# Kernel optimization log

Measured on AMD Instinct MI355X. Metric: run time of the kernel, lower is better.

Reference implementation:

```python
import jax, jax.numpy as jnp
import numpy as np

B, T, C = 2, 4096, 768
N_HEAD = 12
HEAD_DIM = C // N_HEAD


def setup_inputs() -> dict:
    key = jax.random.key(0)
    k1, k2, k3, k4, k5 = jax.random.split(key, 5)
    scale = 1.0 / np.sqrt(C)
    x = jax.random.normal(k1, (B, T, C), dtype=jnp.float32)
    # weights stored as [in, out] (transpose of torch Linear weight)
    W_attn = jax.random.normal(k2, (C, 3 * C), dtype=jnp.float32) * scale
    b_attn = jax.random.normal(k3, (3 * C,), dtype=jnp.float32) * 0.01
    W_proj = jax.random.normal(k4, (C, C), dtype=jnp.float32) * scale
    b_proj = jax.random.normal(k5, (C,), dtype=jnp.float32) * 0.01
    return {"x": x, "W_attn": W_attn, "b_attn": b_attn, "W_proj": W_proj, "b_proj": b_proj}


def reference(x, W_attn, b_attn, W_proj, b_proj):
    Bq, Tq, Cq = x.shape
    qkv = x @ W_attn + b_attn                      # [B, T, 3C]
    q, k, v = jnp.split(qkv, 3, axis=-1)           # each [B, T, C]

    def heads(t):
        return t.reshape(Bq, Tq, N_HEAD, HEAD_DIM).transpose(0, 2, 1, 3)  # [B, H, T, D]

    q, k, v = heads(q), heads(k), heads(v)
    att = jnp.einsum('bhqd,bhkd->bhqk', q, k) * (1.0 / np.sqrt(HEAD_DIM))  # [B, H, T, T]
    causal = jnp.tril(jnp.ones((Tq, Tq), dtype=bool))                      # [T, T]
    att = jnp.where(causal[None, None], att, jnp.finfo(att.dtype).min)
    att = jax.nn.softmax(att, axis=-1)
    y = jnp.einsum('bhqk,bhkd->bhqd', att, v)      # [B, H, T, D]
    y = y.transpose(0, 2, 1, 3).reshape(Bq, Tq, Cq)
    return y @ W_proj + b_proj
```

## Files before the change

kernel.cpp:

```cpp
#include <hip/hip_runtime.h>


#define TSEQ   4096
#define NHEAD  12
#define CDIM   768
#define C3     2304
#define BT_TOT 8192

#define PSTR   72

typedef __bf16 bf16x8 __attribute__((ext_vector_type(8)));
typedef __bf16 bf16x2 __attribute__((ext_vector_type(2)));
typedef float  f32x4  __attribute__((ext_vector_type(4)));

__device__ __forceinline__ unsigned short f2bf(float f) {
  unsigned int u = __builtin_bit_cast(unsigned int, f);
  u += 0x7FFFu + ((u >> 16) & 1u);
  return (unsigned short)(u >> 16);
}

__device__ __forceinline__ unsigned int pack2bf(float a, float b) {
  bf16x2 v = {(__bf16)a, (__bf16)b};
  return __builtin_bit_cast(unsigned int, v);
}

__device__ __forceinline__ f32x4 mfma16(bf16x8 a, bf16x8 b, f32x4 c) {
  return __builtin_amdgcn_mfma_f32_16x16x32_bf16(a, b, c, 0, 0, 0);
}

typedef const __attribute__((address_space(1))) void* gas_ptr;
typedef __attribute__((address_space(3))) void* las_ptr;

#define LGKM_WAIT() __builtin_amdgcn_s_waitcnt(0xC07F)


__global__ __launch_bounds__(256) void cast_f32_bf16(const float* __restrict__ x,
                                                     unsigned short* __restrict__ o, int n) {
  int i = (blockIdx.x * 256 + threadIdx.x) * 4;
  if (i < n) {
    float4 v = *(const float4*)(x + i);
    ushort4 u;
    u.x = f2bf(v.x); u.y = f2bf(v.y); u.z = f2bf(v.z); u.w = f2bf(v.w);
    *(ushort4*)(o + i) = u;
  }
}

__global__ __launch_bounds__(256) void transpose_cast(const float* __restrict__ src,
                                                      unsigned short* __restrict__ dst,
                                                      int K, int N) {
  __shared__ float tile[32][33];
  int n0 = blockIdx.x * 32, k0 = blockIdx.y * 32;
  int tx = threadIdx.x, ty = threadIdx.y;
#pragma unroll
  for (int i = 0; i < 4; ++i)
    tile[ty + i * 8][tx] = src[(size_t)(k0 + ty + i * 8) * N + n0 + tx];
  __syncthreads();
#pragma unroll
  for (int i = 0; i < 4; ++i)
    dst[(size_t)(n0 + ty + i * 8) * K + k0 + tx] = f2bf(tile[tx][ty + i * 8]);
}


__device__ __forceinline__ void gemm_bt_mainloop(const unsigned short* __restrict__ A,
                                                 const unsigned short* __restrict__ BTm,
                                                 int K, int m0, int n0,
                                                 unsigned short* lds, f32x4 acc[4][4]) {
  const int tid = threadIdx.x;
  const int wave = tid >> 6, lane = tid & 63;
  const int quad = lane >> 4, l16 = lane & 15;
  const int wm = (wave >> 1) * 64, wn = (wave & 1) * 64;
  const int srow = tid >> 2;
  const int scol = (tid & 3) * 8;

  for (int k0 = 0; k0 < K; k0 += 32) {
    __syncthreads();
#pragma unroll
    for (int r = 0; r < 2; ++r) {
      const unsigned short* ga = A + (size_t)(m0 + r * 64 + srow) * K + k0 + scol;
      __builtin_amdgcn_global_load_lds((gas_ptr)ga,
          (las_ptr)(lds + r * 2048 + wave * 512), 16, 0, 0);
      const unsigned short* gb = BTm + (size_t)(n0 + r * 64 + srow) * K + k0 + scol;
      __builtin_amdgcn_global_load_lds((gas_ptr)gb,
          (las_ptr)(lds + 4096 + r * 2048 + wave * 512), 16, 0, 0);
    }
    __syncthreads();

    bf16x8 af[4], bfr[4];
#pragma unroll
    for (int i = 0; i < 4; ++i) {
      af[i]  = *(const bf16x8*)(lds + (wm + i * 16 + l16) * 32 + quad * 8);
      bfr[i] = *(const bf16x8*)(lds + 4096 + (wn + i * 16 + l16) * 32 + quad * 8);
    }
#pragma unroll
    for (int i = 0; i < 4; ++i)
#pragma unroll
      for (int j = 0; j < 4; ++j)
        acc[i][j] = mfma16(af[i], bfr[j], acc[i][j]);
  }
}

__global__ __launch_bounds__(256) void gemm_qkv_kernel(
    const unsigned short* __restrict__ A, const unsigned short* __restrict__ BTm,
    const float* __restrict__ bias,
    unsigned short* __restrict__ qbuf, unsigned short* __restrict__ kbuf,
    unsigned short* __restrict__ vtbuf) {
  __shared__ __align__(16) unsigned short lds[128 * 136];
  f32x4 zero = {0.f, 0.f, 0.f, 0.f};
  f32x4 acc[4][4];
#pragma unroll
  for (int i = 0; i < 4; ++i)
#pragma unroll
    for (int j = 0; j < 4; ++j) acc[i][j] = zero;

  const int m0 = blockIdx.y * 128, n0 = blockIdx.x * 128;
  gemm_bt_mainloop(A, BTm, CDIM, m0, n0, lds, acc);

  const int tid = threadIdx.x;
  const int wave = tid >> 6, lane = tid & 63;
  const int quad = lane >> 4, l16 = lane & 15;
  const int wm = (wave >> 1) * 64, wn = (wave & 1) * 64;
  const float KSCALE = 0.125f * 1.44269504088896340736f;

  const int seg = n0 / CDIM;
  const float mult = (seg == 1) ? KSCALE : 1.0f;

  __syncthreads();
#pragma unroll
  for (int j = 0; j < 4; ++j) {
    const int nl = wn + j * 16 + l16;
    const float bv = bias[n0 + nl];
#pragma unroll
    for (int i = 0; i < 4; ++i) {
#pragma unroll
      for (int r = 0; r < 4; ++r) {
        const int ml = wm + i * 16 + quad * 4 + r;
        unsigned short val = f2bf((acc[i][j][r] + bv) * mult);
        if (seg < 2) lds[ml * 136 + nl] = val;
        else         lds[nl * 136 + ml] = val;
      }
    }
  }
  __syncthreads();

  const int row = tid >> 1, half = tid & 1;
  const unsigned short* src = lds + row * 136 + half * 64;
  unsigned short* dst;
  if (seg < 2) {
    const int m = m0 + row, b = m >> 12, t = m & (TSEQ - 1);
    const int nn = (n0 - seg * CDIM) + half * 64;
    const int h = nn >> 6;
    unsigned short* base = (seg == 0) ? qbuf : kbuf;
    dst = base + ((size_t)(b * NHEAD + h) * TSEQ + t) * 64;
  } else {
    const int nn = (n0 - 2 * CDIM) + row;
    const int h = nn >> 6, d = nn & 63;
    const int b = m0 >> 12, t0 = (m0 & (TSEQ - 1)) + half * 64;
    dst = vtbuf + ((size_t)(b * NHEAD + h) * 64 + d) * TSEQ + t0;
  }
#pragma unroll
  for (int k = 0; k < 8; ++k)
    *(uint4*)(dst + k * 8) = *(const uint4*)(src + k * 8);
}

__global__ __launch_bounds__(256) void gemm_out_kernel(
    const unsigned short* __restrict__ A, const unsigned short* __restrict__ BTm,
    const float* __restrict__ bias, float* __restrict__ out) {
  __shared__ __align__(16) unsigned short lds[8192];
  f32x4 zero = {0.f, 0.f, 0.f, 0.f};
  f32x4 acc[4][4];
#pragma unroll
  for (int i = 0; i < 4; ++i)
#pragma unroll
    for (int j = 0; j < 4; ++j) acc[i][j] = zero;

  const int m0 = blockIdx.y * 128, n0 = blockIdx.x * 128;
  gemm_bt_mainloop(A, BTm, CDIM, m0, n0, lds, acc);

  const int tid = threadIdx.x;
  const int wave = tid >> 6, lane = tid & 63;
  const int quad = lane >> 4, l16 = lane & 15;
  const int wm = (wave >> 1) * 64, wn = (wave & 1) * 64;

#pragma unroll
  for (int j = 0; j < 4; ++j) {
    int n = n0 + wn + j * 16 + l16;
    float bv = bias[n];
#pragma unroll
    for (int i = 0; i < 4; ++i) {
#pragma unroll
      for (int r = 0; r < 4; ++r) {
        int m = m0 + wm + i * 16 + quad * 4 + r;
        out[(size_t)m * CDIM + n] = acc[i][j][r] + bv;
      }
    }
  }
}


__device__ __forceinline__ void stage_kv4(const unsigned short* __restrict__ Kp,
                                          const unsigned short* __restrict__ Vp,
                                          int j0, unsigned short* kb, unsigned short* vb,
                                          int tid, int wave) {
  const int row = tid >> 3;
  const int col = ((tid & 7) ^ (row & 7)) * 8;
  __builtin_amdgcn_global_load_lds((gas_ptr)(Kp + (size_t)(j0 + row) * 64 + col),
                                   (las_ptr)(kb + wave * 512), 16, 0, 0);
  __builtin_amdgcn_global_load_lds((gas_ptr)(Kp + (size_t)(j0 + 32 + row) * 64 + col),
                                   (las_ptr)(kb + 2048 + wave * 512), 16, 0, 0);
  __builtin_amdgcn_global_load_lds((gas_ptr)(Vp + (size_t)row * TSEQ + j0 + col),
                                   (las_ptr)(vb + wave * 512), 16, 0, 0);
  __builtin_amdgcn_global_load_lds((gas_ptr)(Vp + (size_t)(row + 32) * TSEQ + j0 + col),
                                   (las_ptr)(vb + 2048 + wave * 512), 16, 0, 0);
}

__device__ __forceinline__ void qk_score(const bf16x8 kf[8], const bf16x8 qf[2], f32x4 s[4]) {
  f32x4 zero = {0.f, 0.f, 0.f, 0.f};
#pragma unroll
  for (int i = 0; i < 4; ++i)
    s[i] = mfma16(kf[2 * i + 1], qf[1], mfma16(kf[2 * i], qf[0], zero));
}

template <bool MASKED>
__device__ __forceinline__ void exp_write(const f32x4 s[4], unsigned short* __restrict__ prow,
                                          int j0, int q0, int l16, int quad, float& lsum) {
#pragma unroll
  for (int i = 0; i < 4; ++i) {
    float p[4];
#pragma unroll
    for (int r = 0; r < 4; ++r) {
      p[r] = __builtin_amdgcn_exp2f(s[i][r]);
      if (MASKED) {
        if (j0 + i * 16 + quad * 4 + r > q0 + l16) p[r] = 0.f;
      }
      lsum += p[r];
    }
    uint2 w;
    w.x = pack2bf(p[0], p[1]);
    w.y = pack2bf(p[2], p[3]);
    *(uint2*)(prow + l16 * PSTR + i * 16 + quad * 4) = w;
  }
}

__device__ __forceinline__ void pv8(const unsigned short* __restrict__ vb, int kcol0,
                                    const unsigned short* __restrict__ prow,
                                    int l16, int quad, f32x4 o[4]) {
  bf16x8 pf0 = *(const bf16x8*)(prow + l16 * PSTR + quad * 8);
  bf16x8 pf1 = *(const bf16x8*)(prow + l16 * PSTR + 32 + quad * 8);
#pragma unroll
  for (int dt = 0; dt < 4; ++dt) {
    bf16x8 v0 = *(const bf16x8*)(vb + (16 * dt + l16) * 64 + kcol0);
    bf16x8 v1 = *(const bf16x8*)(vb + (16 * dt + l16) * 64 + (kcol0 ^ 32));
    o[dt] = mfma16(pf1, v1, mfma16(pf0, v0, o[dt]));
  }
}

__global__ __launch_bounds__(256, 3) void attn_kernel(const unsigned short* __restrict__ qbuf,
                                                      const unsigned short* __restrict__ kbuf,
                                                      const unsigned short* __restrict__ vtbuf,
                                                      unsigned short* __restrict__ y) {
  __shared__ __align__(16) unsigned short k_lds[2][64 * 64];
  __shared__ __align__(16) unsigned short v_lds[2][64 * 64];
  __shared__ __align__(16) unsigned short p_lds[4][2][16 * PSTR];

  const int tid = threadIdx.x;
  const int wave = tid >> 6, lane = tid & 63;
  const int quad = lane >> 4, l16 = lane & 15;

  const int bh = blockIdx.x % 24;
  const int p = blockIdx.x / 24;
  const int qA0 = p * 64 + wave * 16;
  const int qB0 = (63 - p) * 64 + wave * 16;

  const unsigned short* Qp = qbuf + (size_t)bh * TSEQ * 64;
  const unsigned short* Kp = kbuf + (size_t)bh * TSEQ * 64;
  const unsigned short* Vp = vtbuf + (size_t)bh * 64 * TSEQ;
  unsigned short* prowA = &p_lds[wave][0][0];
  unsigned short* prowB = &p_lds[wave][1][0];

  bf16x8 qfA[2], qfB[2];
  qfA[0] = *(const bf16x8*)(Qp + (size_t)(qA0 + l16) * 64 + quad * 8);
  qfA[1] = *(const bf16x8*)(Qp + (size_t)(qA0 + l16) * 64 + 32 + quad * 8);
  qfB[0] = *(const bf16x8*)(Qp + (size_t)(qB0 + l16) * 64 + quad * 8);
  qfB[1] = *(const bf16x8*)(Qp + (size_t)(qB0 + l16) * 64 + 32 + quad * 8);

  f32x4 zero = {0.f, 0.f, 0.f, 0.f};
  f32x4 oA[4], oB[4];
#pragma unroll
  for (int dt = 0; dt < 4; ++dt) { oA[dt] = zero; oB[dt] = zero; }
  float lsA = 0.f, lsB = 0.f;

  const int kcol0 = (quad ^ (l16 & 7)) * 8;
  const int ntiles = 64 - p;

  stage_kv4(Kp, Vp, 0, k_lds[0], v_lds[0], tid, wave);

  for (int jt = 0; jt < ntiles; ++jt) {
    __syncthreads();
    if (jt + 1 < ntiles)
      stage_kv4(Kp, Vp, (jt + 1) * 64, k_lds[(jt + 1) & 1], v_lds[(jt + 1) & 1], tid, wave);

    const unsigned short* kb = k_lds[jt & 1];
    const unsigned short* vb = v_lds[jt & 1];
    const int j0 = jt * 64;
    const bool actA = jt <= p;

    bf16x8 kf[8];
#pragma unroll
    for (int i = 0; i < 4; ++i) {
      kf[2 * i]     = *(const bf16x8*)(kb + (16 * i + l16) * 64 + kcol0);
      kf[2 * i + 1] = *(const bf16x8*)(kb + (16 * i + l16) * 64 + (kcol0 ^ 32));
    }

    f32x4 sA[4], sB[4];
    if (actA) {
      qk_score(kf, qfA, sA);
      if (jt == p) exp_write<true>(sA, prowA, j0, qA0, l16, quad, lsA);
      else         exp_write<false>(sA, prowA, j0, qA0, l16, quad, lsA);
    }
    qk_score(kf, qfB, sB);
    if (jt == ntiles - 1) exp_write<true>(sB, prowB, j0, qB0, l16, quad, lsB);
    else                  exp_write<false>(sB, prowB, j0, qB0, l16, quad, lsB);

    LGKM_WAIT();

    if (actA) pv8(vb, kcol0, prowA, l16, quad, oA);
    pv8(vb, kcol0, prowB, l16, quad, oB);
  }

  lsA += __shfl_xor(lsA, 16); lsA += __shfl_xor(lsA, 32);
  lsB += __shfl_xor(lsB, 16); lsB += __shfl_xor(lsB, 32);

  const int b = bh / NHEAD, h = bh - b * NHEAD;
#pragma unroll
  for (int r = 0; r < 4; ++r) {
    const int qrow = quad * 4 + r;
    float lqA = __shfl(lsA, (lane & 48) + qrow);
    float lqB = __shfl(lsB, (lane & 48) + qrow);
    float invA = 1.0f / lqA, invB = 1.0f / lqB;
    size_t rowA = (size_t)(b * TSEQ + qA0 + qrow) * CDIM + h * 64;
    size_t rowB = (size_t)(b * TSEQ + qB0 + qrow) * CDIM + h * 64;
#pragma unroll
    for (int dt = 0; dt < 4; ++dt) {
      y[rowA + dt * 16 + l16] = f2bf(oA[dt][r] * invA);
      y[rowB + dt * 16 + l16] = f2bf(oB[dt][r] * invB);
    }
  }
}


extern "C" void kernel_launch(void* const* d_in, const int* in_sizes, int n_in,
                              void* d_out, int out_size, void* d_ws, size_t ws_size,
                              hipStream_t stream) {
  const float* x      = (const float*)d_in[0];
  const float* W_attn = (const float*)d_in[1];
  const float* b_attn = (const float*)d_in[2];
  const float* W_proj = (const float*)d_in[3];
  const float* b_proj = (const float*)d_in[4];
  float* out = (float*)d_out;

  unsigned short* xb    = (unsigned short*)d_ws;
  unsigned short* WaT   = xb + (size_t)BT_TOT * CDIM;
  unsigned short* WpT   = WaT + (size_t)C3 * CDIM;
  unsigned short* qbuf  = WpT + (size_t)CDIM * CDIM;
  unsigned short* kbuf  = qbuf + (size_t)2 * NHEAD * TSEQ * 64;
  unsigned short* vtbuf = kbuf + (size_t)2 * NHEAD * TSEQ * 64;
  unsigned short* ybuf  = xb;

  cast_f32_bf16<<<(BT_TOT * CDIM) / 1024, 256, 0, stream>>>(x, xb, BT_TOT * CDIM);
  transpose_cast<<<dim3(C3 / 32, CDIM / 32), dim3(32, 8), 0, stream>>>(W_attn, WaT, CDIM, C3);
  transpose_cast<<<dim3(CDIM / 32, CDIM / 32), dim3(32, 8), 0, stream>>>(W_proj, WpT, CDIM, CDIM);

  gemm_qkv_kernel<<<dim3(C3 / 128, BT_TOT / 128), 256, 0, stream>>>(xb, WaT, b_attn,
                                                                    qbuf, kbuf, vtbuf);
  attn_kernel<<<dim3(24 * 32), 256, 0, stream>>>(qbuf, kbuf, vtbuf, ybuf);
  gemm_out_kernel<<<dim3(CDIM / 128, BT_TOT / 128), 256, 0, stream>>>(ybuf, WpT, b_proj, out);
}
```

Baseline: 239.0 us.

## Split paired query tiles across 8 waves in attention kernel

The attention block grows from 256 to 512 threads. Waves 0-3 now handle the low query tile and waves 4-7 the high tile, where before each wave processed both. K/V staging is spread over twice as many threads, with one load of each per thread. This doubles wave-level parallelism and halves per-wave register use, but the A waves sit idle at barriers after their last tile, and the larger blocks may lower occupancy.

```diff
diff --git a/kernel.cpp b/kernel.cpp
--- a/kernel.cpp
+++ b/kernel.cpp
@@ -197,20 +197,16 @@
 }
 
 
-__device__ __forceinline__ void stage_kv4(const unsigned short* __restrict__ Kp,
-                                          const unsigned short* __restrict__ Vp,
-                                          int j0, unsigned short* kb, unsigned short* vb,
-                                          int tid, int wave) {
+__device__ __forceinline__ void stage_kv(const unsigned short* __restrict__ Kp,
+                                         const unsigned short* __restrict__ Vp,
+                                         int j0, unsigned short* kb, unsigned short* vb,
+                                         int tid, int wave) {
   const int row = tid >> 3;
   const int col = ((tid & 7) ^ (row & 7)) * 8;
   __builtin_amdgcn_global_load_lds((gas_ptr)(Kp + (size_t)(j0 + row) * 64 + col),
                                    (las_ptr)(kb + wave * 512), 16, 0, 0);
-  __builtin_amdgcn_global_load_lds((gas_ptr)(Kp + (size_t)(j0 + 32 + row) * 64 + col),
-                                   (las_ptr)(kb + 2048 + wave * 512), 16, 0, 0);
   __builtin_amdgcn_global_load_lds((gas_ptr)(Vp + (size_t)row * TSEQ + j0 + col),
                                    (las_ptr)(vb + wave * 512), 16, 0, 0);
-  __builtin_amdgcn_global_load_lds((gas_ptr)(Vp + (size_t)(row + 32) * TSEQ + j0 + col),
-                                   (las_ptr)(vb + 2048 + wave * 512), 16, 0, 0);
 }
 
 __device__ __forceinline__ void qk_score(const bf16x8 kf[8], const bf16x8 qf[2], f32x4 s[4]) {
@@ -254,13 +250,13 @@
   }
 }
 
-__global__ __launch_bounds__(256, 3) void attn_kernel(const unsigned short* __restrict__ qbuf,
+__global__ __launch_bounds__(512, 3) void attn_kernel(const unsigned short* __restrict__ qbuf,
                                                       const unsigned short* __restrict__ kbuf,
                                                       const unsigned short* __restrict__ vtbuf,
                                                       unsigned short* __restrict__ y) {
   __shared__ __align__(16) unsigned short k_lds[2][64 * 64];
   __shared__ __align__(16) unsigned short v_lds[2][64 * 64];
-  __shared__ __align__(16) unsigned short p_lds[4][2][16 * PSTR];
+  __shared__ __align__(16) unsigned short p_lds[8][16 * PSTR];
 
   const int tid = threadIdx.x;
   const int wave = tid >> 6, lane = tid & 63;
@@ -268,82 +264,71 @@
 
   const int bh = blockIdx.x % 24;
   const int p = blockIdx.x / 24;
-  const int qA0 = p * 64 + wave * 16;
-  const int qB0 = (63 - p) * 64 + wave * 16;
+  const bool isA = wave < 4;
+  const int qtile = isA ? p : (63 - p);
+  const int q0 = qtile * 64 + (wave & 3) * 16;
 
   const unsigned short* Qp = qbuf + (size_t)bh * TSEQ * 64;
   const unsigned short* Kp = kbuf + (size_t)bh * TSEQ * 64;
   const unsigned short* Vp = vtbuf + (size_t)bh * 64 * TSEQ;
-  unsigned short* prowA = &p_lds[wave][0][0];
-  unsigned short* prowB = &p_lds[wave][1][0];
-
-  bf16x8 qfA[2], qfB[2];
-  qfA[0] = *(const bf16x8*)(Qp + (size_t)(qA0 + l16) * 64 + quad * 8);
-  qfA[1] = *(const bf16x8*)(Qp + (size_t)(qA0 + l16) * 64 + 32 + quad * 8);
-  qfB[0] = *(const bf16x8*)(Qp + (size_t)(qB0 + l16) * 64 + quad * 8);
-  qfB[1] = *(const bf16x8*)(Qp + (size_t)(qB0 + l16) * 64 + 32 + quad * 8);
+  unsigned short* prow = &p_lds[wave][0];
+
+  bf16x8 qf[2];
+  qf[0] = *(const bf16x8*)(Qp + (size_t)(q0 + l16) * 64 + quad * 8);
+  qf[1] = *(const bf16x8*)(Qp + (size_t)(q0 + l16) * 64 + 32 + quad * 8);
 
   f32x4 zero = {0.f, 0.f, 0.f, 0.f};
-  f32x4 oA[4], oB[4];
-#pragma unroll
-  for (int dt = 0; dt < 4; ++dt) { oA[dt] = zero; oB[dt] = zero; }
-  float lsA = 0.f, lsB = 0.f;
+  f32x4 o[4];
+#pragma unroll
+  for (int dt = 0; dt < 4; ++dt) o[dt] = zero;
+  float ls = 0.f;
 
   const int kcol0 = (quad ^ (l16 & 7)) * 8;
   const int ntiles = 64 - p;
-
-  stage_kv4(Kp, Vp, 0, k_lds[0], v_lds[0], tid, wave);
+  const int lasttile = isA ? p : (ntiles - 1);
+
+  stage_kv(Kp, Vp, 0, k_lds[0], v_lds[0], tid, wave);
 
   for (int jt = 0; jt < ntiles; ++jt) {
     __syncthreads();
     if (jt + 1 < ntiles)
-      stage_kv4(Kp, Vp, (jt + 1) * 64, k_lds[(jt + 1) & 1], v_lds[(jt + 1) & 1], tid, wave);
-
-    const unsigned short* kb = k_lds[jt & 1];
-    const unsigned short* vb = v_lds[jt & 1];
-    const int j0 = jt * 64;
-    const bool actA = jt <= p;
-
-    bf16x8 kf[8];
-#pragma unroll
-    for (int i = 0; i < 4; ++i) {
-      kf[2 * i]     = *(const bf16x8*)(kb + (16 * i + l16) * 64 + kcol0);
-      kf[2 * i + 1] = *(const bf16x8*)(kb + (16 * i + l16) * 64 + (kcol0 ^ 32));
-    }
-
-    f32x4 sA[4], sB[4];
-    if (actA) {
-      qk_score(kf, qfA, sA);
-      if (jt == p) exp_write<true>(sA, prowA, j0, qA0, l16, quad, lsA);
-      else         exp_write<false>(sA, prowA, j0, qA0, l16, quad, lsA);
-    }
-    qk_score(kf, qfB, sB);
-    if (jt == ntiles - 1) exp_write<true>(sB, prowB, j0, qB0, l16, quad, lsB);
-    else                  exp_write<false>(sB, prowB, j0, qB0, l16, quad, lsB);
-
-    LGKM_WAIT();
-
-    if (actA) pv8(vb, kcol0, prowA, l16, quad, oA);
-    pv8(vb, kcol0, prowB, l16, quad, oB);
-  }
-
-  lsA += __shfl_xor(lsA, 16); lsA += __shfl_xor(lsA, 32);
-  lsB += __shfl_xor(lsB, 16); lsB += __shfl_xor(lsB, 32);
+      stage_kv(Kp, Vp, (jt + 1) * 64, k_lds[(jt + 1) & 1], v_lds[(jt + 1) & 1], tid, wave);
+
+    if (jt <= lasttile) {
+      const unsigned short* kb = k_lds[jt & 1];
+      const unsigned short* vb = v_lds[jt & 1];
+      const int j0 = jt * 64;
+
+      bf16x8 kf[8];
+#pragma unroll
+      for (int i = 0; i < 4; ++i) {
+        kf[2 * i]     = *(const bf16x8*)(kb + (16 * i + l16) * 64 + kcol0);
+        kf[2 * i + 1] = *(const bf16x8*)(kb + (16 * i + l16) * 64 + (kcol0 ^ 32));
+      }
+
+      f32x4 s[4];
+      qk_score(kf, qf, s);
+      if (jt == lasttile) exp_write<true>(s, prow, j0, q0, l16, quad, ls);
+      else                exp_write<false>(s, prow, j0, q0, l16, quad, ls);
+
+      LGKM_WAIT();
+
+      pv8(vb, kcol0, prow, l16, quad, o);
+    }
+  }
+
+  ls += __shfl_xor(ls, 16); ls += __shfl_xor(ls, 32);
 
   const int b = bh / NHEAD, h = bh - b * NHEAD;
 #pragma unroll
   for (int r = 0; r < 4; ++r) {
     const int qrow = quad * 4 + r;
-    float lqA = __shfl(lsA, (lane & 48) + qrow);
-    float lqB = __shfl(lsB, (lane & 48) + qrow);
-    float invA = 1.0f / lqA, invB = 1.0f / lqB;
-    size_t rowA = (size_t)(b * TSEQ + qA0 + qrow) * CDIM + h * 64;
-    size_t rowB = (size_t)(b * TSEQ + qB0 + qrow) * CDIM + h * 64;
-#pragma unroll
-    for (int dt = 0; dt < 4; ++dt) {
-      y[rowA + dt * 16 + l16] = f2bf(oA[dt][r] * invA);
-      y[rowB + dt * 16 + l16] = f2bf(oB[dt][r] * invB);
-    }
+    float lq = __shfl(ls, (lane & 48) + qrow);
+    float inv = 1.0f / lq;
+    size_t row = (size_t)(b * TSEQ + q0 + qrow) * CDIM + h * 64;
+#pragma unroll
+    for (int dt = 0; dt < 4; ++dt)
+      y[row + dt * 16 + l16] = f2bf(o[dt][r] * inv);
   }
 }
 
@@ -372,6 +357,6 @@
 
   gemm_qkv_kernel<<<dim3(C3 / 128, BT_TOT / 128), 256, 0, stream>>>(xb, WaT, b_attn,
                                                                     qbuf, kbuf, vtbuf);
-  attn_kernel<<<dim3(24 * 32), 256, 0, stream>>>(qbuf, kbuf, vtbuf, ybuf);
+  attn_kernel<<<dim3(24 * 32), 512, 0, stream>>>(qbuf, kbuf, vtbuf, ybuf);
   gemm_out_kernel<<<dim3(CDIM / 128, BT_TOT / 128), 256, 0, stream>>>(ybuf, WpT, b_proj, out);
 }
```

Measured after the change: 234.4 us. No clear change (-1.9%).

## Reassign waves so each handles 32 rows of one query tile

Applied to the files above, without the earlier changes.

Previously each of the four waves processed 16 rows from a short tile A and 16 rows from a long tile B. Now waves 0-1 take the short tile and waves 2-3 the long tile, with 32 contiguous rows each, so the V fragments loaded for PV are shared across two MFMA chains. Waves on the short tile skip compute once past their last tile and only join the barriers and staging. This concentrates work on waves 2-3, which creates per-wave load imbalance inside the block but lets waves 0-1 go idle early and frees issue slots for co-resident blocks.

```diff
diff --git a/kernel.cpp b/kernel.cpp
--- a/kernel.cpp
+++ b/kernel.cpp
@@ -241,16 +241,20 @@
   }
 }
 
-__device__ __forceinline__ void pv8(const unsigned short* __restrict__ vb, int kcol0,
-                                    const unsigned short* __restrict__ prow,
-                                    int l16, int quad, f32x4 o[4]) {
-  bf16x8 pf0 = *(const bf16x8*)(prow + l16 * PSTR + quad * 8);
-  bf16x8 pf1 = *(const bf16x8*)(prow + l16 * PSTR + 32 + quad * 8);
+__device__ __forceinline__ void pv_dual(const unsigned short* __restrict__ vb, int kcol0,
+                                        const unsigned short* __restrict__ p0,
+                                        const unsigned short* __restrict__ p1,
+                                        int l16, int quad, f32x4 o0[4], f32x4 o1[4]) {
+  bf16x8 a00 = *(const bf16x8*)(p0 + l16 * PSTR + quad * 8);
+  bf16x8 a01 = *(const bf16x8*)(p0 + l16 * PSTR + 32 + quad * 8);
+  bf16x8 a10 = *(const bf16x8*)(p1 + l16 * PSTR + quad * 8);
+  bf16x8 a11 = *(const bf16x8*)(p1 + l16 * PSTR + 32 + quad * 8);
 #pragma unroll
   for (int dt = 0; dt < 4; ++dt) {
     bf16x8 v0 = *(const bf16x8*)(vb + (16 * dt + l16) * 64 + kcol0);
     bf16x8 v1 = *(const bf16x8*)(vb + (16 * dt + l16) * 64 + (kcol0 ^ 32));
-    o[dt] = mfma16(pf1, v1, mfma16(pf0, v0, o[dt]));
+    o0[dt] = mfma16(a01, v1, mfma16(a00, v0, o0[dt]));
+    o1[dt] = mfma16(a11, v1, mfma16(a10, v0, o1[dt]));
   }
 }
 
@@ -268,29 +272,31 @@
 
   const int bh = blockIdx.x % 24;
   const int p = blockIdx.x / 24;
-  const int qA0 = p * 64 + wave * 16;
-  const int qB0 = (63 - p) * 64 + wave * 16;
+  const bool isA = wave < 2;
+  const int qtile = isA ? p : (63 - p);
+  const int q0 = qtile * 64 + (wave & 1) * 32;
 
   const unsigned short* Qp = qbuf + (size_t)bh * TSEQ * 64;
   const unsigned short* Kp = kbuf + (size_t)bh * TSEQ * 64;
   const unsigned short* Vp = vtbuf + (size_t)bh * 64 * TSEQ;
-  unsigned short* prowA = &p_lds[wave][0][0];
-  unsigned short* prowB = &p_lds[wave][1][0];
-
-  bf16x8 qfA[2], qfB[2];
-  qfA[0] = *(const bf16x8*)(Qp + (size_t)(qA0 + l16) * 64 + quad * 8);
-  qfA[1] = *(const bf16x8*)(Qp + (size_t)(qA0 + l16) * 64 + 32 + quad * 8);
-  qfB[0] = *(const bf16x8*)(Qp + (size_t)(qB0 + l16) * 64 + quad * 8);
-  qfB[1] = *(const bf16x8*)(Qp + (size_t)(qB0 + l16) * 64 + 32 + quad * 8);
+  unsigned short* prow0 = &p_lds[wave][0][0];
+  unsigned short* prow1 = &p_lds[wave][1][0];
+
+  bf16x8 qf0[2], qf1[2];
+  qf0[0] = *(const bf16x8*)(Qp + (size_t)(q0 + l16) * 64 + quad * 8);
+  qf0[1] = *(const bf16x8*)(Qp + (size_t)(q0 + l16) * 64 + 32 + quad * 8);
+  qf1[0] = *(const bf16x8*)(Qp + (size_t)(q0 + 16 + l16) * 64 + quad * 8);
+  qf1[1] = *(const bf16x8*)(Qp + (size_t)(q0 + 16 + l16) * 64 + 32 + quad * 8);
 
   f32x4 zero = {0.f, 0.f, 0.f, 0.f};
-  f32x4 oA[4], oB[4];
-#pragma unroll
-  for (int dt = 0; dt < 4; ++dt) { oA[dt] = zero; oB[dt] = zero; }
-  float lsA = 0.f, lsB = 0.f;
+  f32x4 o0[4], o1[4];
+#pragma unroll
+  for (int dt = 0; dt < 4; ++dt) { o0[dt] = zero; o1[dt] = zero; }
+  float ls0 = 0.f, ls1 = 0.f;
 
   const int kcol0 = (quad ^ (l16 & 7)) * 8;
   const int ntiles = 64 - p;
+  const int lasttile = isA ? p : (ntiles - 1);
 
   stage_kv4(Kp, Vp, 0, k_lds[0], v_lds[0], tid, wave);
 
@@ -299,50 +305,51 @@
     if (jt + 1 < ntiles)
       stage_kv4(Kp, Vp, (jt + 1) * 64, k_lds[(jt + 1) & 1], v_lds[(jt + 1) & 1], tid, wave);
 
-    const unsigned short* kb = k_lds[jt & 1];
-    const unsigned short* vb = v_lds[jt & 1];
-    const int j0 = jt * 64;
-    const bool actA = jt <= p;
-
-    bf16x8 kf[8];
-#pragma unroll
-    for (int i = 0; i < 4; ++i) {
-      kf[2 * i]     = *(const bf16x8*)(kb + (16 * i + l16) * 64 + kcol0);
-      kf[2 * i + 1] = *(const bf16x8*)(kb + (16 * i + l16) * 64 + (kcol0 ^ 32));
-    }
-
-    f32x4 sA[4], sB[4];
-    if (actA) {
-      qk_score(kf, qfA, sA);
-      if (jt == p) exp_write<true>(sA, prowA, j0, qA0, l16, quad, lsA);
-      else         exp_write<false>(sA, prowA, j0, qA0, l16, quad, lsA);
-    }
-    qk_score(kf, qfB, sB);
-    if (jt == ntiles - 1) exp_write<true>(sB, prowB, j0, qB0, l16, quad, lsB);
-    else                  exp_write<false>(sB, prowB, j0, qB0, l16, quad, lsB);
-
-    LGKM_WAIT();
-
-    if (actA) pv8(vb, kcol0, prowA, l16, quad, oA);
-    pv8(vb, kcol0, prowB, l16, quad, oB);
-  }
-
-  lsA += __shfl_xor(lsA, 16); lsA += __shfl_xor(lsA, 32);
-  lsB += __shfl_xor(lsB, 16); lsB += __shfl_xor(lsB, 32);
+    if (jt <= lasttile) {
+      const unsigned short* kb = k_lds[jt & 1];
+      const unsigned short* vb = v_lds[jt & 1];
+      const int j0 = jt * 64;
+
+      bf16x8 kf[8];
+#pragma unroll
+      for (int i = 0; i < 4; ++i) {
+        kf[2 * i]     = *(const bf16x8*)(kb + (16 * i + l16) * 64 + kcol0);
+        kf[2 * i + 1] = *(const bf16x8*)(kb + (16 * i + l16) * 64 + (kcol0 ^ 32));
+      }
+
+      f32x4 s0[4], s1[4];
+      qk_score(kf, qf0, s0);
+      qk_score(kf, qf1, s1);
+      if (jt == lasttile) {
+        exp_write<true>(s0, prow0, j0, q0,      l16, quad, ls0);
+        exp_write<true>(s1, prow1, j0, q0 + 16, l16, quad, ls1);
+      } else {
+        exp_write<false>(s0, prow0, j0, q0,      l16, quad, ls0);
+        exp_write<false>(s1, prow1, j0, q0 + 16, l16, quad, ls1);
+      }
+
+      LGKM_WAIT();
+
+      pv_dual(vb, kcol0, prow0, prow1, l16, quad, o0, o1);
+    }
+  }
+
+  ls0 += __shfl_xor(ls0, 16); ls0 += __shfl_xor(ls0, 32);
+  ls1 += __shfl_xor(ls1, 16); ls1 += __shfl_xor(ls1, 32);
 
   const int b = bh / NHEAD, h = bh - b * NHEAD;
 #pragma unroll
   for (int r = 0; r < 4; ++r) {
     const int qrow = quad * 4 + r;
-    float lqA = __shfl(lsA, (lane & 48) + qrow);
-    float lqB = __shfl(lsB, (lane & 48) + qrow);
-    float invA = 1.0f / lqA, invB = 1.0f / lqB;
-    size_t rowA = (size_t)(b * TSEQ + qA0 + qrow) * CDIM + h * 64;
-    size_t rowB = (size_t)(b * TSEQ + qB0 + qrow) * CDIM + h * 64;
+    float lq0 = __shfl(ls0, (lane & 48) + qrow);
+    float lq1 = __shfl(ls1, (lane & 48) + qrow);
+    float inv0 = 1.0f / lq0, inv1 = 1.0f / lq1;
+    size_t row0 = (size_t)(b * TSEQ + q0 + qrow) * CDIM + h * 64;
+    size_t row1 = (size_t)(b * TSEQ + q0 + 16 + qrow) * CDIM + h * 64;
 #pragma unroll
     for (int dt = 0; dt < 4; ++dt) {
-      y[rowA + dt * 16 + l16] = f2bf(oA[dt][r] * invA);
-      y[rowB + dt * 16 + l16] = f2bf(oB[dt][r] * invB);
+      y[row0 + dt * 16 + l16] = f2bf(o0[dt][r] * inv0);
+      y[row1 + dt * 16 + l16] = f2bf(o1[dt][r] * inv1);
     }
   }
 }
```

Measured after the change: 246.1 us. 3.0% more time.
